# Kernel optimization log

Hardware: AMD Instinct MI355X
Metric: run time of the kernel (lower is better)

Reference implementation:

```python
import jax, jax.numpy as jnp
import numpy as np

N_NODES = 100000
N_EDGES = 1600000
NFEAT = 128
NHID = 128
NCLASS = 40


def setup_inputs() -> dict:
    key = jax.random.key(0)
    ks = jax.random.split(key, 8)
    x = jax.random.normal(ks[0], (N_NODES, NFEAT), dtype=jnp.float32)
    edge_index = jax.random.randint(ks[1], (2, N_EDGES), 0, N_NODES, dtype=jnp.int64 if jax.config.read('jax_enable_x64') else jnp.int32)
    edge_weight = jax.random.uniform(ks[2], (N_EDGES,), dtype=jnp.float32)
    s = 1.0 / np.sqrt(NFEAT)
    W1 = jax.random.normal(ks[3], (NFEAT, NHID), dtype=jnp.float32) * s
    b1 = jnp.zeros((NHID,), dtype=jnp.float32)
    W2 = jax.random.normal(ks[4], (NHID, NHID), dtype=jnp.float32) * s
    b2 = jnp.zeros((NHID,), dtype=jnp.float32)
    Wfc = jax.random.normal(ks[5], (2 * NHID, NCLASS), dtype=jnp.float32) * (1.0 / np.sqrt(2 * NHID))
    bfc = jnp.zeros((NCLASS,), dtype=jnp.float32)
    return {"x": x, "edge_index": edge_index, "edge_weight": edge_weight,
            "W1": W1, "b1": b1, "W2": W2, "b2": b2, "Wfc": Wfc, "bfc": bfc}


def _gin_layer(h, src, dst, edge_weight, W, b, n_nodes):
    # GINConv (eps=0): nn((1+eps)*h + sum_{j in N(i)} w_ij * h_j), nn = Linear+ReLU
    msgs = edge_weight[:, None] * h[src]                      # [E, D] gather
    agg = jax.ops.segment_sum(msgs, dst, num_segments=n_nodes)  # [N, D] scatter-add
    z = (h + agg) @ W + b
    # outer F.relu(gc(.)) composed with the Sequential's ReLU is a single relu
    return jax.nn.relu(z)


def reference(x, edge_index, edge_weight, W1, b1, W2, b2, Wfc, bfc):
    n = x.shape[0]
    src, dst = edge_index[0], edge_index[1]
    x1 = _gin_layer(x, src, dst, edge_weight, W1, b1, n)   # [N, NHID]
    x2 = _gin_layer(x1, src, dst, edge_weight, W2, b2, n)  # [N, NHID]
    x_last = jnp.concatenate([x1, x2], axis=1)             # JumpingKnowledge 'cat'
    logits = x_last @ Wfc + bfc                            # [N, NCLASS]
    return jax.nn.log_softmax(logits, axis=1)
```

## Files before the change

### kernel.cpp

```cpp
#include <hip/hip_runtime.h>
#include <math.h>

#define NCLS 40
#define BSZ 32
#define BCAP 768
#define CSTR 16

using f16x8 = __attribute__((ext_vector_type(8))) _Float16;
using f16x2 = __attribute__((ext_vector_type(2))) _Float16;
using f32x4 = __attribute__((ext_vector_type(4))) float;

__global__ void init_cur(int* __restrict__ bcur, int nbk) {
  int i = blockIdx.x * 256 + threadIdx.x;
  if (i < nbk) bcur[i * CSTR] = i * BCAP;
}

__global__ __launch_bounds__(256) void append_part(const int* __restrict__ ei,
    const float* __restrict__ ew, int* __restrict__ bcur,
    int2* __restrict__ bedge, int e) {
  int part = blockIdx.x & 7;
  int grp = blockIdx.x >> 3;
  int ngrp = gridDim.x >> 3;
  for (int i = grp * 256 + threadIdx.x; i < e; i += ngrp * 256) {
    int d = ei[e + i];
    int b = d >> 5;
    if ((b & 7) == part) {
      int slot = atomicAdd(&bcur[b * CSTR], 1);
      if (slot < b * BCAP + BCAP)
        bedge[slot] = make_int2(ei[i] | ((d & 31) << 20), __float_as_int(ew[i]));
    }
  }
}

__global__ void bucket_count(const int* __restrict__ bcur, int* __restrict__ cntb, int nbk) {
  int i = blockIdx.x * 256 + threadIdx.x;
  if (i < nbk) cntb[i] = min(bcur[i * CSTR] - i * BCAP, BCAP);
}

__global__ __launch_bounds__(1024) void scan_block(const int* __restrict__ src,
    int* __restrict__ dst, int* __restrict__ partials, int n) {
  __shared__ int s[1024];
  int t = threadIdx.x;
  int i = blockIdx.x * 1024 + t;
  int v = (i < n) ? src[i] : 0;
  s[t] = v;
  __syncthreads();
  int val = v;
  for (int d = 1; d < 1024; d <<= 1) {
    int other = (t >= d) ? s[t - d] : 0;
    __syncthreads();
    val += other;
    s[t] = val;
    __syncthreads();
  }
  if (i < n) dst[i] = val - v;
  if (t == 1023) partials[blockIdx.x] = val;
}

__global__ __launch_bounds__(128) void scan_partials(int* __restrict__ partials, int nb) {
  __shared__ int s[128];
  int t = threadIdx.x;
  int v = (t < nb) ? partials[t] : 0;
  s[t] = v;
  __syncthreads();
  int val = v;
  for (int d = 1; d < 128; d <<= 1) {
    int other = (t >= d) ? s[t - d] : 0;
    __syncthreads();
    val += other;
    s[t] = val;
    __syncthreads();
  }
  if (t < nb) partials[t] = val - v;
}

__global__ void scan_add_b(int* __restrict__ dst, const int* __restrict__ partials, int n) {
  int i = blockIdx.x * 256 + threadIdx.x;
  if (i < n) dst[i] += partials[i >> 10];
}

__global__ __launch_bounds__(256) void bucket2csr(const int* __restrict__ bcur,
    const int2* __restrict__ bedge, const int* __restrict__ bbase,
    int* __restrict__ offs, int2* __restrict__ cedge, int nbk, int n, int e) {
  __shared__ int2 tmp[BCAP];
  __shared__ int hist[BSZ], lpref[BSZ], cur[BSZ];
  int t = threadIdx.x;
  int b = blockIdx.x;
  int cnt = min(bcur[b * CSTR] - b * BCAP, BCAP);
  int base = bbase[b];
  if (t < BSZ) hist[t] = 0;
  __syncthreads();
  for (int i = t; i < cnt; i += 256)
    atomicAdd(&hist[(unsigned)bedge[b * BCAP + i].x >> 20], 1);
  __syncthreads();
  if (t == 0) {
    int a = 0;
    #pragma unroll
    for (int j = 0; j < BSZ; j++) { int v = hist[j]; lpref[j] = a; cur[j] = a; a += v; }
  }
  __syncthreads();
  for (int i = t; i < cnt; i += 256) {
    int2 r = bedge[b * BCAP + i];
    int dl = (unsigned)r.x >> 20;
    int pos = atomicAdd(&cur[dl], 1);
    tmp[pos] = make_int2(r.x & 0xFFFFF, r.y);
  }
  __syncthreads();
  for (int i = t; i < cnt; i += 256)
    cedge[base + i] = tmp[i];
  if (t < BSZ && b * BSZ + t < n) offs[b * BSZ + t] = base + lpref[t];
  if (b == nbk - 1 && t == 0) offs[n] = base + cnt;
}

__global__ void convert_wt(const float* __restrict__ W, _Float16* __restrict__ Wt) {
  int c = blockIdx.x;
  int k = threadIdx.x;
  Wt[c * 128 + k] = (_Float16)W[k * 128 + c];
}

template<bool A32>
__global__ __launch_bounds__(256) void gemm_f16(const void* __restrict__ Av,
    const _Float16* __restrict__ Wt, _Float16* __restrict__ Y, int n) {
  __shared__ _Float16 Ys[64][136];
  int t = threadIdx.x;
  int wv = t >> 6, l = t & 63;
  int r0 = blockIdx.x * 64 + wv * 16;
  int arow = r0 + (l & 15);
  int kq = (l >> 4) * 8;
  bool rowok = arow < n;
  f32x4 acc[8] = {};
  for (int kc = 0; kc < 128; kc += 32) {
    f16x8 a = {};
    if (rowok) {
      if constexpr (A32) {
        const float* xp = (const float*)Av + (size_t)arow * 128 + kc + kq;
        float4 u0 = *(const float4*)xp;
        float4 u1 = *(const float4*)(xp + 4);
        a[0] = (_Float16)u0.x; a[1] = (_Float16)u0.y;
        a[2] = (_Float16)u0.z; a[3] = (_Float16)u0.w;
        a[4] = (_Float16)u1.x; a[5] = (_Float16)u1.y;
        a[6] = (_Float16)u1.z; a[7] = (_Float16)u1.w;
      } else {
        a = *(const f16x8*)((const _Float16*)Av + (size_t)arow * 128 + kc + kq);
      }
    }
    #pragma unroll
    for (int j = 0; j < 8; j++) {
      f16x8 b = *(const f16x8*)(Wt + (size_t)(j * 16 + (l & 15)) * 128 + kc + kq);
      acc[j] = __builtin_amdgcn_mfma_f32_16x16x32_f16(a, b, acc[j], 0, 0, 0);
    }
  }
  #pragma unroll
  for (int j = 0; j < 8; j++)
    #pragma unroll
    for (int i = 0; i < 4; i++)
      Ys[wv * 16 + (l >> 4) * 4 + i][j * 16 + (l & 15)] = (_Float16)acc[j][i];
  __syncthreads();
  int r = t >> 2;
  int c0 = (t & 3) * 32;
  int grow = blockIdx.x * 64 + r;
  if (grow < n) {
    #pragma unroll
    for (int i = 0; i < 4; i++) {
      f16x8 v = *(const f16x8*)&Ys[r][c0 + i * 8];
      *(f16x8*)(Y + (size_t)grow * 128 + c0 + i * 8) = v;
    }
  }
}

__global__ __launch_bounds__(256) void spmm_relu_f16(const _Float16* __restrict__ Y,
    const int* __restrict__ offs, const int2* __restrict__ cedge,
    const float* __restrict__ bias, _Float16* __restrict__ H, int n) {
  int wv = threadIdx.x >> 6;
  int lane = threadIdx.x & 63;
  int node = blockIdx.x * 4 + wv;
  if (node >= n) return;
  int c = lane * 2;
  const _Float16* Yc = Y + c;
  int e0 = offs[node], e1 = offs[node + 1];
  float ax0 = 0.f, ay0 = 0.f, ax1 = 0.f, ay1 = 0.f;
  float ax2 = 0.f, ay2 = 0.f, ax3 = 0.f, ay3 = 0.f;
  int e = e0;
  for (; e + 3 < e1; e += 4) {
    int2 p0 = cedge[e];
    int2 p1 = cedge[e + 1];
    int2 p2 = cedge[e + 2];
    int2 p3 = cedge[e + 3];
    f16x2 v0 = *(const f16x2*)(Yc + (size_t)p0.x * 128);
    f16x2 v1 = *(const f16x2*)(Yc + (size_t)p1.x * 128);
    f16x2 v2 = *(const f16x2*)(Yc + (size_t)p2.x * 128);
    f16x2 v3 = *(const f16x2*)(Yc + (size_t)p3.x * 128);
    float w0 = __int_as_float(p0.y), w1 = __int_as_float(p1.y);
    float w2 = __int_as_float(p2.y), w3 = __int_as_float(p3.y);
    ax0 = fmaf(w0, (float)v0.x, ax0); ay0 = fmaf(w0, (float)v0.y, ay0);
    ax1 = fmaf(w1, (float)v1.x, ax1); ay1 = fmaf(w1, (float)v1.y, ay1);
    ax2 = fmaf(w2, (float)v2.x, ax2); ay2 = fmaf(w2, (float)v2.y, ay2);
    ax3 = fmaf(w3, (float)v3.x, ax3); ay3 = fmaf(w3, (float)v3.y, ay3);
  }
  for (; e < e1; e++) {
    int2 p0 = cedge[e];
    f16x2 v0 = *(const f16x2*)(Yc + (size_t)p0.x * 128);
    float w0 = __int_as_float(p0.y);
    ax0 = fmaf(w0, (float)v0.x, ax0); ay0 = fmaf(w0, (float)v0.y, ay0);
  }
  f16x2 yv = *(const f16x2*)(Yc + (size_t)node * 128);
  float2 bv = *(const float2*)(bias + c);
  float zx = (float)yv.x + (ax0 + ax1) + (ax2 + ax3) + bv.x;
  float zy = (float)yv.y + (ay0 + ay1) + (ay2 + ay3) + bv.y;
  f16x2 o;
  o.x = (_Float16)fmaxf(zx, 0.f);
  o.y = (_Float16)fmaxf(zy, 0.f);
  *(f16x2*)(H + (size_t)node * 128 + c) = o;
}

__global__ __launch_bounds__(256) void fc_lsm(const _Float16* __restrict__ H1,
    const _Float16* __restrict__ H2, const float* __restrict__ Wfc,
    const float* __restrict__ bfc, float* __restrict__ out, int n) {
  __shared__ float Wl[256 * NCLS];
  __shared__ float Hs[64][132];
  int t = threadIdx.x;
  for (int i = t; i < 256 * NCLS; i += 256) Wl[i] = Wfc[i];
  int tx = t & 7, ty = t >> 3;
  int row0 = blockIdx.x * 128;
  float acc[4][5] = {};
  for (int kc = 0; kc < 256; kc += 64) {
    {
      int r = t & 127;
      int half = t >> 7;
      int row = row0 + r;
      const _Float16* src = (kc < 128)
          ? (H1 + (size_t)row * 128 + kc + half * 32)
          : (H2 + (size_t)row * 128 + (kc - 128) + half * 32);
      if (row < n) {
        #pragma unroll
        for (int i = 0; i < 4; i++) {
          f16x8 v = ((const f16x8*)src)[i];
          #pragma unroll
          for (int q = 0; q < 8; q++) Hs[half * 32 + i * 8 + q][r] = (float)v[q];
        }
      } else {
        #pragma unroll
        for (int k = 0; k < 32; k++) Hs[half * 32 + k][r] = 0.f;
      }
    }
    __syncthreads();
    #pragma unroll 4
    for (int k = 0; k < 64; k++) {
      float4 a = *(const float4*)&Hs[k][ty * 4];
      const float* wrow = &Wl[(kc + k) * NCLS + tx * 5];
      float b_[5];
      #pragma unroll
      for (int j = 0; j < 5; j++) b_[j] = wrow[j];
      #pragma unroll
      for (int j = 0; j < 5; j++) {
        acc[0][j] = fmaf(a.x, b_[j], acc[0][j]);
        acc[1][j] = fmaf(a.y, b_[j], acc[1][j]);
        acc[2][j] = fmaf(a.z, b_[j], acc[2][j]);
        acc[3][j] = fmaf(a.w, b_[j], acc[3][j]);
      }
    }
    __syncthreads();
  }
  int c0 = tx * 5;
  float bv[5];
  #pragma unroll
  for (int j = 0; j < 5; j++) bv[j] = bfc[c0 + j];
  #pragma unroll
  for (int i = 0; i < 4; i++) {
    float lg[5];
    #pragma unroll
    for (int j = 0; j < 5; j++) lg[j] = acc[i][j] + bv[j];
    float m = lg[0];
    #pragma unroll
    for (int j = 1; j < 5; j++) m = fmaxf(m, lg[j]);
    m = fmaxf(m, __shfl_xor(m, 1));
    m = fmaxf(m, __shfl_xor(m, 2));
    m = fmaxf(m, __shfl_xor(m, 4));
    float ssum = 0.f;
    #pragma unroll
    for (int j = 0; j < 5; j++) ssum += __expf(lg[j] - m);
    ssum += __shfl_xor(ssum, 1);
    ssum += __shfl_xor(ssum, 2);
    ssum += __shfl_xor(ssum, 4);
    float lse = m + __logf(ssum);
    int row = row0 + ty * 4 + i;
    if (row < n) {
      #pragma unroll
      for (int j = 0; j < 5; j++) out[(size_t)row * NCLS + c0 + j] = lg[j] - lse;
    }
  }
}

extern "C" void kernel_launch(void* const* d_in, const int* in_sizes, int n_in,
                              void* d_out, int out_size, void* d_ws, size_t ws_size,
                              hipStream_t stream) {
  const float* x   = (const float*)d_in[0];
  const int*   ei  = (const int*)d_in[1];
  const float* ew  = (const float*)d_in[2];
  const float* W1  = (const float*)d_in[3];
  const float* b1  = (const float*)d_in[4];
  const float* W2  = (const float*)d_in[5];
  const float* b2  = (const float*)d_in[6];
  const float* Wfc = (const float*)d_in[7];
  const float* bfc = (const float*)d_in[8];
  float* out = (float*)d_out;
  int n = in_sizes[0] / 128;
  int e = in_sizes[2];
  int nbk = (n + BSZ - 1) / BSZ;

  char* ws = (char*)d_ws;
  size_t off = 0;
  auto alloc = [&](size_t bytes) -> void* {
    void* p = ws + off; off += (bytes + 255) & ~(size_t)255; return p;
  };
  int*      bcur  = (int*)alloc((size_t)nbk * CSTR * 4);
  int*      cntb  = (int*)alloc((size_t)nbk * 4);
  int*      bbase = (int*)alloc((size_t)nbk * 4);
  int*      parts = (int*)alloc(1024 * 4);
  int*      offs  = (int*)alloc((size_t)(n + 1) * 4);
  int2*     bedge = (int2*)alloc((size_t)nbk * BCAP * 8);
  int2*     cedge = (int2*)alloc((size_t)e * 8);
  _Float16* w1t   = (_Float16*)alloc(128 * 128 * 2);
  _Float16* w2t   = (_Float16*)alloc(128 * 128 * 2);
  _Float16* y     = (_Float16*)alloc((size_t)n * 128 * 2);
  _Float16* h1    = (_Float16*)alloc((size_t)n * 128 * 2);
  _Float16* h2    = (_Float16*)alloc((size_t)n * 128 * 2);

  int nbb = (nbk + 1023) / 1024;

  init_cur<<<(nbk + 255) / 256, 256, 0, stream>>>(bcur, nbk);
  append_part<<<8 * 104, 256, 0, stream>>>(ei, ew, bcur, bedge, e);
  bucket_count<<<(nbk + 255) / 256, 256, 0, stream>>>(bcur, cntb, nbk);
  scan_block<<<nbb, 1024, 0, stream>>>(cntb, bbase, parts, nbk);
  scan_partials<<<1, 128, 0, stream>>>(parts, nbb);
  scan_add_b<<<(nbk + 255) / 256, 256, 0, stream>>>(bbase, parts, nbk);
  bucket2csr<<<nbk, 256, 0, stream>>>(bcur, bedge, bbase, offs, cedge, nbk, n, e);

  convert_wt<<<128, 128, 0, stream>>>(W1, w1t);
  convert_wt<<<128, 128, 0, stream>>>(W2, w2t);

  int gb = (n + 63) / 64;
  gemm_f16<true><<<gb, 256, 0, stream>>>((const void*)x, w1t, y, n);
  spmm_relu_f16<<<(n + 3) / 4, 256, 0, stream>>>(y, offs, cedge, b1, h1, n);
  gemm_f16<false><<<gb, 256, 0, stream>>>((const void*)h1, w2t, y, n);
  spmm_relu_f16<<<(n + 3) / 4, 256, 0, stream>>>(y, offs, cedge, b2, h2, n);
  fc_lsm<<<(n + 127) / 128, 256, 0, stream>>>(h1, h2, Wfc, bfc, out, n);
}
```

Before: 492.5 us.

## Fuse per-bucket sort into SpMM and drop CSR build and scan kernels

Removes the separate bucket-count, three-stage scan and bucket-to-CSR kernels. Each SpMM block now sorts its destination bucket's edges in shared memory and aggregates its 32 nodes straight from there. This saves five launches and a full write and re-read of the CSR edge array. In exchange the bucket sort is redone in both SpMM passes, and each wave now handles 8 nodes in sequence, which lowers parallelism. The append kernel's grid is also widened.

Measured after the change: 438.6 us. 11.0% less time.

```diff
diff --git a/kernel.cpp b/kernel.cpp
--- a/kernel.cpp
+++ b/kernel.cpp
@@ -30,86 +30,6 @@
         bedge[slot] = make_int2(ei[i] | ((d & 31) << 20), __float_as_int(ew[i]));
     }
   }
-}
-
-__global__ void bucket_count(const int* __restrict__ bcur, int* __restrict__ cntb, int nbk) {
-  int i = blockIdx.x * 256 + threadIdx.x;
-  if (i < nbk) cntb[i] = min(bcur[i * CSTR] - i * BCAP, BCAP);
-}
-
-__global__ __launch_bounds__(1024) void scan_block(const int* __restrict__ src,
-    int* __restrict__ dst, int* __restrict__ partials, int n) {
-  __shared__ int s[1024];
-  int t = threadIdx.x;
-  int i = blockIdx.x * 1024 + t;
-  int v = (i < n) ? src[i] : 0;
-  s[t] = v;
-  __syncthreads();
-  int val = v;
-  for (int d = 1; d < 1024; d <<= 1) {
-    int other = (t >= d) ? s[t - d] : 0;
-    __syncthreads();
-    val += other;
-    s[t] = val;
-    __syncthreads();
-  }
-  if (i < n) dst[i] = val - v;
-  if (t == 1023) partials[blockIdx.x] = val;
-}
-
-__global__ __launch_bounds__(128) void scan_partials(int* __restrict__ partials, int nb) {
-  __shared__ int s[128];
-  int t = threadIdx.x;
-  int v = (t < nb) ? partials[t] : 0;
-  s[t] = v;
-  __syncthreads();
-  int val = v;
-  for (int d = 1; d < 128; d <<= 1) {
-    int other = (t >= d) ? s[t - d] : 0;
-    __syncthreads();
-    val += other;
-    s[t] = val;
-    __syncthreads();
-  }
-  if (t < nb) partials[t] = val - v;
-}
-
-__global__ void scan_add_b(int* __restrict__ dst, const int* __restrict__ partials, int n) {
-  int i = blockIdx.x * 256 + threadIdx.x;
-  if (i < n) dst[i] += partials[i >> 10];
-}
-
-__global__ __launch_bounds__(256) void bucket2csr(const int* __restrict__ bcur,
-    const int2* __restrict__ bedge, const int* __restrict__ bbase,
-    int* __restrict__ offs, int2* __restrict__ cedge, int nbk, int n, int e) {
-  __shared__ int2 tmp[BCAP];
-  __shared__ int hist[BSZ], lpref[BSZ], cur[BSZ];
-  int t = threadIdx.x;
-  int b = blockIdx.x;
-  int cnt = min(bcur[b * CSTR] - b * BCAP, BCAP);
-  int base = bbase[b];
-  if (t < BSZ) hist[t] = 0;
-  __syncthreads();
-  for (int i = t; i < cnt; i += 256)
-    atomicAdd(&hist[(unsigned)bedge[b * BCAP + i].x >> 20], 1);
-  __syncthreads();
-  if (t == 0) {
-    int a = 0;
-    #pragma unroll
-    for (int j = 0; j < BSZ; j++) { int v = hist[j]; lpref[j] = a; cur[j] = a; a += v; }
-  }
-  __syncthreads();
-  for (int i = t; i < cnt; i += 256) {
-    int2 r = bedge[b * BCAP + i];
-    int dl = (unsigned)r.x >> 20;
-    int pos = atomicAdd(&cur[dl], 1);
-    tmp[pos] = make_int2(r.x & 0xFFFFF, r.y);
-  }
-  __syncthreads();
-  for (int i = t; i < cnt; i += 256)
-    cedge[base + i] = tmp[i];
-  if (t < BSZ && b * BSZ + t < n) offs[b * BSZ + t] = base + lpref[t];
-  if (b == nbk - 1 && t == 0) offs[n] = base + cnt;
 }
 
 __global__ void convert_wt(const float* __restrict__ W, _Float16* __restrict__ Wt) {
@@ -168,49 +88,72 @@
   }
 }
 
-__global__ __launch_bounds__(256) void spmm_relu_f16(const _Float16* __restrict__ Y,
-    const int* __restrict__ offs, const int2* __restrict__ cedge,
+__global__ __launch_bounds__(256) void spmm_sort_relu(const _Float16* __restrict__ Y,
+    const int* __restrict__ bcur, const int2* __restrict__ bedge,
     const float* __restrict__ bias, _Float16* __restrict__ H, int n) {
-  int wv = threadIdx.x >> 6;
-  int lane = threadIdx.x & 63;
-  int node = blockIdx.x * 4 + wv;
-  if (node >= n) return;
+  __shared__ int2 tmp[BCAP];
+  __shared__ int hist[BSZ], lpref[BSZ + 1], cur[BSZ];
+  int t = threadIdx.x;
+  int b = blockIdx.x;
+  int cnt = min(bcur[b * CSTR] - b * BCAP, BCAP);
+  if (t < BSZ) hist[t] = 0;
+  __syncthreads();
+  for (int i = t; i < cnt; i += 256)
+    atomicAdd(&hist[(unsigned)bedge[b * BCAP + i].x >> 20], 1);
+  __syncthreads();
+  if (t == 0) {
+    int a = 0;
+    #pragma unroll
+    for (int j = 0; j < BSZ; j++) { int v = hist[j]; lpref[j] = a; cur[j] = a; a += v; }
+    lpref[BSZ] = a;
+  }
+  __syncthreads();
+  for (int i = t; i < cnt; i += 256) {
+    int2 r = bedge[b * BCAP + i];
+    int dl = (unsigned)r.x >> 20;
+    int pos = atomicAdd(&cur[dl], 1);
+    tmp[pos] = make_int2(r.x & 0xFFFFF, r.y);
+  }
+  __syncthreads();
+  int wv = t >> 6, lane = t & 63;
   int c = lane * 2;
   const _Float16* Yc = Y + c;
-  int e0 = offs[node], e1 = offs[node + 1];
-  float ax0 = 0.f, ay0 = 0.f, ax1 = 0.f, ay1 = 0.f;
-  float ax2 = 0.f, ay2 = 0.f, ax3 = 0.f, ay3 = 0.f;
-  int e = e0;
-  for (; e + 3 < e1; e += 4) {
-    int2 p0 = cedge[e];
-    int2 p1 = cedge[e + 1];
-    int2 p2 = cedge[e + 2];
-    int2 p3 = cedge[e + 3];
-    f16x2 v0 = *(const f16x2*)(Yc + (size_t)p0.x * 128);
-    f16x2 v1 = *(const f16x2*)(Yc + (size_t)p1.x * 128);
-    f16x2 v2 = *(const f16x2*)(Yc + (size_t)p2.x * 128);
-    f16x2 v3 = *(const f16x2*)(Yc + (size_t)p3.x * 128);
-    float w0 = __int_as_float(p0.y), w1 = __int_as_float(p1.y);
-    float w2 = __int_as_float(p2.y), w3 = __int_as_float(p3.y);
-    ax0 = fmaf(w0, (float)v0.x, ax0); ay0 = fmaf(w0, (float)v0.y, ay0);
-    ax1 = fmaf(w1, (float)v1.x, ax1); ay1 = fmaf(w1, (float)v1.y, ay1);
-    ax2 = fmaf(w2, (float)v2.x, ax2); ay2 = fmaf(w2, (float)v2.y, ay2);
-    ax3 = fmaf(w3, (float)v3.x, ax3); ay3 = fmaf(w3, (float)v3.y, ay3);
-  }
-  for (; e < e1; e++) {
-    int2 p0 = cedge[e];
-    f16x2 v0 = *(const f16x2*)(Yc + (size_t)p0.x * 128);
-    float w0 = __int_as_float(p0.y);
-    ax0 = fmaf(w0, (float)v0.x, ax0); ay0 = fmaf(w0, (float)v0.y, ay0);
-  }
-  f16x2 yv = *(const f16x2*)(Yc + (size_t)node * 128);
-  float2 bv = *(const float2*)(bias + c);
-  float zx = (float)yv.x + (ax0 + ax1) + (ax2 + ax3) + bv.x;
-  float zy = (float)yv.y + (ay0 + ay1) + (ay2 + ay3) + bv.y;
-  f16x2 o;
-  o.x = (_Float16)fmaxf(zx, 0.f);
-  o.y = (_Float16)fmaxf(zy, 0.f);
-  *(f16x2*)(H + (size_t)node * 128 + c) = o;
+  for (int q = 0; q < 8; q++) {
+    int dl = wv * 8 + q;
+    int node = b * BSZ + dl;
+    if (node >= n) continue;
+    int e0 = lpref[dl], e1 = lpref[dl + 1];
+    float ax0 = 0.f, ay0 = 0.f, ax1 = 0.f, ay1 = 0.f;
+    float ax2 = 0.f, ay2 = 0.f, ax3 = 0.f, ay3 = 0.f;
+    int e = e0;
+    for (; e + 3 < e1; e += 4) {
+      int2 p0 = tmp[e], p1 = tmp[e + 1], p2 = tmp[e + 2], p3 = tmp[e + 3];
+      f16x2 v0 = *(const f16x2*)(Yc + (size_t)p0.x * 128);
+      f16x2 v1 = *(const f16x2*)(Yc + (size_t)p1.x * 128);
+      f16x2 v2 = *(const f16x2*)(Yc + (size_t)p2.x * 128);
+      f16x2 v3 = *(const f16x2*)(Yc + (size_t)p3.x * 128);
+      float w0 = __int_as_float(p0.y), w1 = __int_as_float(p1.y);
+      float w2 = __int_as_float(p2.y), w3 = __int_as_float(p3.y);
+      ax0 = fmaf(w0, (float)v0.x, ax0); ay0 = fmaf(w0, (float)v0.y, ay0);
+      ax1 = fmaf(w1, (float)v1.x, ax1); ay1 = fmaf(w1, (float)v1.y, ay1);
+      ax2 = fmaf(w2, (float)v2.x, ax2); ay2 = fmaf(w2, (float)v2.y, ay2);
+      ax3 = fmaf(w3, (float)v3.x, ax3); ay3 = fmaf(w3, (float)v3.y, ay3);
+    }
+    for (; e < e1; e++) {
+      int2 p0 = tmp[e];
+      f16x2 v0 = *(const f16x2*)(Yc + (size_t)p0.x * 128);
+      float w0 = __int_as_float(p0.y);
+      ax0 = fmaf(w0, (float)v0.x, ax0); ay0 = fmaf(w0, (float)v0.y, ay0);
+    }
+    f16x2 yv = *(const f16x2*)(Yc + (size_t)node * 128);
+    float2 bv = *(const float2*)(bias + c);
+    float zx = (float)yv.x + (ax0 + ax1) + (ax2 + ax3) + bv.x;
+    float zy = (float)yv.y + (ay0 + ay1) + (ay2 + ay3) + bv.y;
+    f16x2 o;
+    o.x = (_Float16)fmaxf(zx, 0.f);
+    o.y = (_Float16)fmaxf(zy, 0.f);
+    *(f16x2*)(H + (size_t)node * 128 + c) = o;
+  }
 }
 
 __global__ __launch_bounds__(256) void fc_lsm(const _Float16* __restrict__ H1,
@@ -314,35 +257,23 @@
     void* p = ws + off; off += (bytes + 255) & ~(size_t)255; return p;
   };
   int*      bcur  = (int*)alloc((size_t)nbk * CSTR * 4);
-  int*      cntb  = (int*)alloc((size_t)nbk * 4);
-  int*      bbase = (int*)alloc((size_t)nbk * 4);
-  int*      parts = (int*)alloc(1024 * 4);
-  int*      offs  = (int*)alloc((size_t)(n + 1) * 4);
   int2*     bedge = (int2*)alloc((size_t)nbk * BCAP * 8);
-  int2*     cedge = (int2*)alloc((size_t)e * 8);
   _Float16* w1t   = (_Float16*)alloc(128 * 128 * 2);
   _Float16* w2t   = (_Float16*)alloc(128 * 128 * 2);
   _Float16* y     = (_Float16*)alloc((size_t)n * 128 * 2);
   _Float16* h1    = (_Float16*)alloc((size_t)n * 128 * 2);
   _Float16* h2    = (_Float16*)alloc((size_t)n * 128 * 2);
 
-  int nbb = (nbk + 1023) / 1024;
-
   init_cur<<<(nbk + 255) / 256, 256, 0, stream>>>(bcur, nbk);
-  append_part<<<8 * 104, 256, 0, stream>>>(ei, ew, bcur, bedge, e);
-  bucket_count<<<(nbk + 255) / 256, 256, 0, stream>>>(bcur, cntb, nbk);
-  scan_block<<<nbb, 1024, 0, stream>>>(cntb, bbase, parts, nbk);
-  scan_partials<<<1, 128, 0, stream>>>(parts, nbb);
-  scan_add_b<<<(nbk + 255) / 256, 256, 0, stream>>>(bbase, parts, nbk);
-  bucket2csr<<<nbk, 256, 0, stream>>>(bcur, bedge, bbase, offs, cedge, nbk, n, e);
+  append_part<<<8 * 256, 256, 0, stream>>>(ei, ew, bcur, bedge, e);
 
   convert_wt<<<128, 128, 0, stream>>>(W1, w1t);
   convert_wt<<<128, 128, 0, stream>>>(W2, w2t);
 
   int gb = (n + 63) / 64;
   gemm_f16<true><<<gb, 256, 0, stream>>>((const void*)x, w1t, y, n);
-  spmm_relu_f16<<<(n + 3) / 4, 256, 0, stream>>>(y, offs, cedge, b1, h1, n);
+  spmm_sort_relu<<<nbk, 256, 0, stream>>>(y, bcur, bedge, b1, h1, n);
   gemm_f16<false><<<gb, 256, 0, stream>>>((const void*)h1, w2t, y, n);
-  spmm_relu_f16<<<(n + 3) / 4, 256, 0, stream>>>(y, offs, cedge, b2, h2, n);
+  spmm_sort_relu<<<nbk, 256, 0, stream>>>(y, bcur, bedge, b2, h2, n);
   fc_lsm<<<(n + 127) / 128, 256, 0, stream>>>(h1, h2, Wfc, bfc, out, n);
 }
```
